# Performance work log

Measured on AMD Instinct MI355X. Metric: run time of the kernel, lower is better.

## Reference

```python
import jax, jax.numpy as jnp
import numpy as np

N, E = 20000, 320000
C, IN_NF, HID_NF, OUT_NF, CH_NF, RAD_NF = 14, 128, 128, 128, 16, 128
CONSTANT = 1.0
LN_EPS = 1e-5
SCALE = 0.02


def _pool_matrix(c, dtype):
    # RollerPooling buffer: pool_matrix[i] averages a sliding window of size c-i
    ones = np.ones((c, c), dtype=np.float32)
    mats = [(np.triu(ones) - np.triu(ones, k=c - i)) / float(c - i) for i in range(c)]
    return jnp.asarray(np.stack(mats), dtype=dtype)


def setup_inputs() -> dict:
    key = jax.random.key(0)
    ks = jax.random.split(key, 32)
    h = jax.random.normal(ks[0], (N, IN_NF), jnp.float32)
    x = jax.random.normal(ks[1], (N, C, 3), jnp.float32)
    row = jax.random.randint(ks[2], (E,), 0, N)
    off = jax.random.randint(ks[3], (E,), 1, N)
    col = (row + off) % N  # guarantees row != col (avoids zero-distance edges)
    channel_attr = jax.random.normal(ks[4], (N, C, CH_NF), jnp.float32)
    w = jax.random.uniform(ks[5], (N, C), jnp.float32, 0.1, 1.0)
    keep = jax.random.uniform(ks[6], (N, C)) > 0.3
    keep = keep.at[:, 0].set(True)  # every node has >=1 active channel
    channel_weights = w * keep.astype(jnp.float32)

    def lin(k, o, i):
        k1, k2 = jax.random.split(k)
        return (jax.random.normal(k1, (o, i), jnp.float32) * SCALE,
                jax.random.normal(k2, (o,), jnp.float32) * SCALE)

    radial_W, radial_b = lin(ks[7], RAD_NF, CH_NF * CH_NF)
    e1_W, e1_b = lin(ks[8], HID_NF, 2 * IN_NF + RAD_NF)
    e2_W, e2_b = lin(ks[9], HID_NF, HID_NF)
    att_W, att_b = lin(ks[10], 1, HID_NF)
    c1_W, c1_b = lin(ks[11], HID_NF, HID_NF)
    c2_W, c2_b = lin(ks[12], C, HID_NF)
    n1_W, n1_b = lin(ks[13], HID_NF, IN_NF + HID_NF)
    n2_W, n2_b = lin(ks[14], OUT_NF, HID_NF)
    ln_g = jnp.ones((OUT_NF,), jnp.float32)
    ln_b = jnp.zeros((OUT_NF,), jnp.float32)
    return dict(h=h, x=x, row=row, col=col, channel_attr=channel_attr,
                channel_weights=channel_weights,
                radial_W=radial_W, radial_b=radial_b,
                e1_W=e1_W, e1_b=e1_b, e2_W=e2_W, e2_b=e2_b,
                att_W=att_W, att_b=att_b,
                c1_W=c1_W, c1_b=c1_b, c2_W=c2_W, c2_b=c2_b,
                n1_W=n1_W, n1_b=n1_b, n2_W=n2_W, n2_b=n2_b,
                ln_g=ln_g, ln_b=ln_b)


def _scatter_mean(v, idx, n):
    s = jnp.zeros((n,) + v.shape[1:], v.dtype).at[idx].add(v)
    cnt = jnp.zeros((n,), v.dtype).at[idx].add(1.0)
    cnt = jnp.maximum(cnt, 1.0)
    return s / cnt.reshape((n,) + (1,) * (v.ndim - 1))


def _forward(h, x, row, col, channel_attr, channel_weights,
             radial_W, radial_b, e1_W, e1_b, e2_W, e2_b, att_W, att_b,
             c1_W, c1_b, c2_W, c2_b, n1_W, n1_b, n2_W, n2_b, ln_g, ln_b):
    n, c, d = x.shape
    silu = jax.nn.silu
    coord_r = x[row]           # [E, C, 3]
    coord_c = x[col]
    # pairwise channel distances [E, C, C]
    dist = jnp.linalg.norm(coord_r[:, :, None, :] - coord_c[:, None, :, :], axis=-1)
    cw_r = channel_weights[row]
    cw_c = channel_weights[col]
    coord_msg = dist * (cw_r[:, :, None] * cw_c[:, None, :])
    # attr_r^T @ coord_msg @ attr_c -> [E, CH_NF, CH_NF]
    radial = jnp.einsum('eca,ecd,edb->eab', channel_attr[row], coord_msg, channel_attr[col])
    radial = radial.reshape(radial.shape[0], -1)
    rnorm = jnp.linalg.norm(radial, axis=-1, keepdims=True) + CONSTANT
    radial = (radial @ radial_W.T + radial_b) / rnorm  # [E, RAD_NF]
    # pooled column coord over active channels
    mask = (channel_weights != 0).astype(x.dtype)      # [N, C]
    csum = mask.sum(-1)                                # [N]
    pooled_col = (coord_c * mask[col][:, :, None]).sum(1) / csum[col][:, None]  # [E, 3]
    coord_diff = coord_r - pooled_col[:, None, :]      # [E, C, 3]
    # edge MLP (dropout = identity in eval)
    ef = jnp.concatenate([h[row], h[col], radial], axis=-1)
    ef = silu(ef @ e1_W.T + e1_b)
    ef = silu(ef @ e2_W.T + e2_b)
    ef = ef * jax.nn.sigmoid(ef @ att_W.T + att_b)     # att_mlp (hidden_nf == input_nf)
    # coord MLP + roller pooling
    ch = silu(ef @ c1_W.T + c1_b) @ c2_W.T + c2_b      # [E, C]
    tsize = csum[row].astype(jnp.int32) - 1            # [E] in [0, C-1]
    pool_mat = _pool_matrix(c, x.dtype)                # [C, C, C]
    pooled = jnp.einsum('eij,ej->ei', pool_mat[tsize], ch)  # [E, C]
    trans = coord_diff * pooled[:, :, None]            # [E, C, 3]
    x_out = x + _scatter_mean(trans, row, n)
    agg = _scatter_mean(ef, col, n)
    nh = jnp.concatenate([h, agg], axis=-1)
    nh = silu(nh @ n1_W.T + n1_b) @ n2_W.T + n2_b
    y = h + nh
    mu = y.mean(-1, keepdims=True)
    var = ((y - mu) ** 2).mean(-1, keepdims=True)
    h_out = (y - mu) / jnp.sqrt(var + LN_EPS) * ln_g + ln_b
    return h_out, x_out


def reference(h, x, row, col, channel_attr, channel_weights,
              radial_W, radial_b, e1_W, e1_b, e2_W, e2_b, att_W, att_b,
              c1_W, c1_b, c2_W, c2_b, n1_W, n1_b, n2_W, n2_b, ln_g, ln_b):
    return _forward(h, x, row, col, channel_attr, channel_weights,
                    radial_W, radial_b, e1_W, e1_b, e2_W, e2_b, att_W, att_b,
                    c1_W, c1_b, c2_W, c2_b, n1_W, n1_b, n2_W, n2_b, ln_g, ln_b)
```

## Files before the change

### kernel.cpp

```cpp
#include <hip/hip_runtime.h>
#include <math.h>

#define NN 20000
#define NE 320000

typedef const float* fp;
typedef short short8 __attribute__((ext_vector_type(8)));
typedef short short4v __attribute__((ext_vector_type(4)));
typedef float f32x4 __attribute__((ext_vector_type(4)));

__device__ __forceinline__ short F2B(float f) {
    unsigned u = __float_as_uint(f);
    return (short)((u + 0x7fffu + ((u >> 16) & 1u)) >> 16);
}
__device__ __forceinline__ short F2Bf(float f) {
    return (short)((__float_as_uint(f) + 0x8000u) >> 16);
}
__device__ __forceinline__ float B2F(short s) {
    return __uint_as_float(((unsigned)(unsigned short)s) << 16);
}
__device__ __forceinline__ float siluf(float v) { return v / (1.f + __expf(-v)); }
__device__ __forceinline__ f32x4 ld4(const float* p) {
    f32x4 v;
    __builtin_memcpy(&v, p, 16);
    return v;
}

#if defined(__has_builtin)
#if __has_builtin(__builtin_amdgcn_mfma_f32_16x16x16bf16_1k)
#define MFMA16_BUILTIN 1
__device__ __forceinline__ f32x4 mfma16(short4v a, short4v b, f32x4 c) {
    return __builtin_amdgcn_mfma_f32_16x16x16bf16_1k(a, b, c, 0, 0, 0);
}
#elif __has_builtin(__builtin_amdgcn_mfma_f32_16x16x16_bf16)
#define MFMA16_BUILTIN 1
__device__ __forceinline__ f32x4 mfma16(short4v a, short4v b, f32x4 c) {
    return __builtin_amdgcn_mfma_f32_16x16x16_bf16(a, b, c, 0, 0, 0);
}
#endif
#endif
#ifndef MFMA16_BUILTIN
__device__ __forceinline__ f32x4 mfma16(short4v a, short4v b, f32x4 c) {
    f32x4 d;
    asm volatile("s_nop 1\n\tv_mfma_f32_16x16x16_bf16 %0, %1, %2, %3\n\ts_nop 7\n\ts_nop 7"
                 : "=v"(d) : "v"(a), "v"(b), "v"(c));
    return d;
}
#endif

__global__ void k_prep_w(fp e1W, fp e2W, fp c1W, fp c2W, fp n1W, fp n2W,
                         short* __restrict__ wb) {
    int i = blockIdx.x * 256 + threadIdx.x;
    if (i >= 149504) return;
    if (i >= 32768 && i < 65536) return;
    float v;
    if (i < 32768)       { int o = i >> 8, k = i & 255; v = e1W[o * 384 + k]; }
    else if (i < 81920)  v = e2W[i - 65536];
    else if (i < 98304)  v = c1W[i - 81920];
    else if (i < 100352) { int q = i - 98304; v = (q < 1792) ? c2W[q] : 0.f; }
    else if (i < 133120) v = n1W[i - 100352];
    else                 v = n2W[i - 133120];
    wb[i] = F2B(v);
}

__global__ void k_fold(fp e1W, fp rW, fp rB, short* __restrict__ wb,
                       float* __restrict__ bc) {
    int o = blockIdx.x, k = threadIdx.x;
    float acc = 0.f;
    for (int m = 0; m < 128; m++) acc += e1W[o * 384 + 256 + m] * rW[m * 256 + k];
    wb[32768 + o * 256 + k] = F2B(acc);
    if (k == 0) {
        float b = 0.f;
        for (int m = 0; m < 128; m++) b += e1W[o * 384 + 256 + m] * rB[m];
        bc[o] = b;
    }
}

__global__ void k_prep_h(fp h, short* __restrict__ hb) {
    int i = blockIdx.x * 256 + threadIdx.x;
    if (i < NN * 128) hb[i] = F2B(h[i]);
}

__global__ void k_prep_attrT(fp attr, fp cw, short* __restrict__ aT) {
    int i = blockIdx.x * 256 + threadIdx.x;
    if (i >= NN * 256) return;
    int n = i >> 8, rem = i & 255, c = rem >> 4, a = rem & 15;
    float v = (c < 14) ? attr[(size_t)n * 224 + c * 16 + a] * cw[n * 14 + c] : 0.f;
    aT[(size_t)n * 256 + a * 16 + c] = F2B(v);
}

__global__ void k_node_pre(fp x, fp cw, float* __restrict__ csum, float* __restrict__ pool) {
    int n = blockIdx.x * blockDim.x + threadIdx.x;
    if (n >= NN) return;
    float cnt = 0.f, px = 0.f, py = 0.f, pz = 0.f;
#pragma unroll
    for (int c = 0; c < 14; c++) {
        float w = cw[n * 14 + c];
        if (w != 0.f) {
            cnt += 1.f;
            px += x[(n * 14 + c) * 3 + 0];
            py += x[(n * 14 + c) * 3 + 1];
            pz += x[(n * 14 + c) * 3 + 2];
        }
    }
    if (cnt < 1.f) cnt = 1.f;
    csum[n] = cnt;
    pool[n * 3 + 0] = px / cnt;
    pool[n * 3 + 1] = py / cnt;
    pool[n * 3 + 2] = pz / cnt;
}

__global__ void k_prep_all(fp e1W, fp e2W, fp c1W, fp c2W, fp n1W, fp n2W,
                           fp rW, fp rB, fp h, fp x, fp attr, fp cw,
                           const int* __restrict__ row, const int* __restrict__ col,
                           short* __restrict__ wb, float* __restrict__ bc,
                           short* __restrict__ hb,
                           float* __restrict__ csum, float* __restrict__ pool,
                           short* __restrict__ aT,
                           int* __restrict__ cnt_r, int* __restrict__ cnt_c) {
    int b = blockIdx.x;
    const int tid = threadIdx.x;
    if (b < 1250) {
        int e = b * 256 + tid;
        if (e < NE) {
            atomicAdd(&cnt_c[col[e]], 1);
            atomicAdd(&cnt_r[row[e]], 1);
        }
        return;
    }
    b -= 1250;
    if (b < 584) {
        int i = b * 256 + tid;
        if (i >= 149504) return;
        if (i >= 32768 && i < 65536) return;
        float v;
        if (i < 32768)       { int o = i >> 8, k = i & 255; v = e1W[o * 384 + k]; }
        else if (i < 81920)  v = e2W[i - 65536];
        else if (i < 98304)  v = c1W[i - 81920];
        else if (i < 100352) { int q = i - 98304; v = (q < 1792) ? c2W[q] : 0.f; }
        else if (i < 133120) v = n1W[i - 100352];
        else                 v = n2W[i - 133120];
        wb[i] = F2B(v);
        return;
    }
    b -= 584;
    if (b < 128) {
        int o = b, k = tid;
        float acc = 0.f;
        for (int m = 0; m < 128; m++) acc += e1W[o * 384 + 256 + m] * rW[m * 256 + k];
        wb[32768 + o * 256 + k] = F2B(acc);
        if (k == 0) {
            float bsum = 0.f;
            for (int m = 0; m < 128; m++) bsum += e1W[o * 384 + 256 + m] * rB[m];
            bc[o] = bsum;
        }
        return;
    }
    b -= 128;
    if (b < 10000) {
        int i = b * 256 + tid;
        hb[i] = F2B(h[i]);
        return;
    }
    b -= 10000;
    if (b < 79) {
        int n = b * 256 + tid;
        if (n >= NN) return;
        float cnt = 0.f, px = 0.f, py = 0.f, pz = 0.f;
#pragma unroll
        for (int c = 0; c < 14; c++) {
            float w = cw[n * 14 + c];
            if (w != 0.f) {
                cnt += 1.f;
                px += x[(n * 14 + c) * 3 + 0];
                py += x[(n * 14 + c) * 3 + 1];
                pz += x[(n * 14 + c) * 3 + 2];
            }
        }
        if (cnt < 1.f) cnt = 1.f;
        csum[n] = cnt;
        pool[n * 3 + 0] = px / cnt;
        pool[n * 3 + 1] = py / cnt;
        pool[n * 3 + 2] = pz / cnt;
        return;
    }
    b -= 79;
    {
        int i = b * 256 + tid;
        int n = i >> 8, rem = i & 255, c = rem >> 4, a = rem & 15;
        float v = (c < 14) ? attr[(size_t)n * 224 + c * 16 + a] * cw[n * 14 + c] : 0.f;
        aT[(size_t)n * 256 + a * 16 + c] = F2B(v);
    }
}

__global__ void k_scan(int* __restrict__ cnt0, int* __restrict__ cnt1,
                       int* __restrict__ off0, int* __restrict__ off1) {
    __shared__ int part[256];
    const int tid = threadIdx.x;
    for (int a = 0; a < 2; a++) {
        int* cnt = a ? cnt1 : cnt0;
        int* off = a ? off1 : off0;
        int c0 = tid * 79, c1 = c0 + 79;
        if (c1 > 20000) c1 = 20000;
        int s = 0;
        for (int i = c0; i < c1; i++) s += cnt[i];
        part[tid] = s;
        __syncthreads();
        if (tid == 0) {
            int r = 0;
            for (int i = 0; i < 256; i++) { int t = part[i]; part[i] = r; r += t; }
        }
        __syncthreads();
        int run = part[tid];
        for (int i = c0; i < c1; i++) {
            int cv = cnt[i];
            off[i] = run;
            cnt[i] = run;
            run += cv;
        }
        if (tid == 255) off[20000] = run;
        __syncthreads();
    }
}

__global__ void k_fill(const int* __restrict__ row, const int* __restrict__ col,
                       int* __restrict__ head_r, int* __restrict__ head_c,
                       int* __restrict__ eidx_r,
                       int* __restrict__ row_s, int* __restrict__ col_s) {
    int e = blockIdx.x * 256 + threadIdx.x;
    if (e >= NE) return;
    int r = row[e], c = col[e];
    int pc = atomicAdd(&head_c[c], 1);
    row_s[pc] = r;
    col_s[pc] = c;
    int pr = atomicAdd(&head_r[r], 1);
    eidx_r[pr] = pc;
}

__device__ __forceinline__ void gemm_lds(const short* __restrict__ A, int sA,
                                         const short* __restrict__ W, int Ws, int K,
                                         int mt, int nt0, int nts, f32x4* acc) {
    const int lane = threadIdx.x & 63;
    const short* ap = A + (mt * 16 + (lane & 15)) * sA + ((lane >> 4) * 8);
    for (int k0 = 0; k0 < K; k0 += 32) {
        short8 a = *(const short8*)(ap + k0);
#pragma unroll
        for (int t = 0; t < nts; t++) {
            short8 b = *(const short8*)(W + ((nt0 + t) * 16 + (lane & 15)) * Ws + k0 + ((lane >> 4) * 8));
            acc[t] = __builtin_amdgcn_mfma_f32_16x16x32_bf16(a, b, acc[t], 0, 0, 0);
        }
    }
}
__device__ __forceinline__ void gemm_grow(const short* __restrict__ arow,
                                          const short* __restrict__ W, int Ws, int K,
                                          int nt0, int nts, f32x4* acc) {
    const int lane = threadIdx.x & 63;
    for (int k0 = 0; k0 < K; k0 += 32) {
        short8 a = *(const short8*)(arow + k0);
#pragma unroll
        for (int t = 0; t < nts; t++) {
            short8 b = *(const short8*)(W + ((nt0 + t) * 16 + (lane & 15)) * Ws + k0 + ((lane >> 4) * 8));
            acc[t] = __builtin_amdgcn_mfma_f32_16x16x32_bf16(a, b, acc[t], 0, 0, 0);
        }
    }
}

__global__ __launch_bounds__(256, 2) void k_hw(const short* __restrict__ hb,
                                               const short* __restrict__ wb,
                                               short* __restrict__ H12) {
    __shared__ __attribute__((aligned(16))) short A[32 * 136];
    const int tid = threadIdx.x, lane = tid & 63, w = tid >> 6;
    const int bb = lane & 15, quad = lane >> 4;
    const int mt = w & 1, nh = w >> 1, nb0 = blockIdx.x * 32;
    for (int p = tid; p < 512; p += 256) {
        int i = p >> 4, v = p & 15;
        *(short8*)(A + i * 136 + v * 8) = *(const short8*)(hb + (size_t)(nb0 + i) * 128 + v * 8);
    }
    __syncthreads();
    f32x4 acc[4];
#pragma unroll
    for (int t = 0; t < 4; t++) acc[t] = (f32x4){0.f, 0.f, 0.f, 0.f};
    gemm_lds(A, 136, wb, 256, 128, mt, nh * 4, 4, acc);
#pragma unroll
    for (int t = 0; t < 4; t++)
#pragma unroll
        for (int i = 0; i < 4; i++) {
            int m = mt * 16 + quad * 4 + i, n = (nh * 4 + t) * 16 + bb;
            H12[(size_t)(nb0 + m) * 256 + n] = F2Bf(acc[t][i]);
        }
#pragma unroll
    for (int t = 0; t < 4; t++) acc[t] = (f32x4){0.f, 0.f, 0.f, 0.f};
    gemm_lds(A, 136, wb + 128, 256, 128, mt, nh * 4, 4, acc);
#pragma unroll
    for (int t = 0; t < 4; t++)
#pragma unroll
        for (int i = 0; i < 4; i++) {
            int m = mt * 16 + quad * 4 + i, n = (nh * 4 + t) * 16 + bb;
            H12[(size_t)(nb0 + m) * 256 + 128 + n] = F2Bf(acc[t][i]);
        }
}

__global__ __launch_bounds__(256, 7) void k_edge(
    fp x, const int* __restrict__ row_s, const int* __restrict__ col_s,
    const short* __restrict__ attrT, const short* __restrict__ H12,
    const short* __restrict__ wb, const float* __restrict__ bc,
    fp e1B, fp e2B, fp aW, fp aB, fp c1B, fp c2B,
    const float* __restrict__ csum, const float* __restrict__ poolc,
    short* __restrict__ e1p, short* __restrict__ pooledb,
    float* __restrict__ pcrec) {
    __shared__ __attribute__((aligned(16))) short U[8704];
    __shared__ float s_inv[32];
    __shared__ int s_r[32], s_c[32];
    __shared__ float s_ch[32][14];
    __shared__ float s_red8[32][8], s_gate[32];

    const int tid = threadIdx.x, lane = tid & 63, w = tid >> 6;
    const int bb = lane & 15, quad = lane >> 4;
    const int mt = w & 1, nh = w >> 1;
    const int e0 = blockIdx.x * 32;
    const short* Wc = wb + 32768;
    short* Ar = U;
    short* V1 = U;
    short* V2 = U + 4352;

    if (tid < 32) { s_r[tid] = row_s[e0 + tid]; s_c[tid] = col_s[e0 + tid]; }
    __syncthreads();

    const int iic = bb < 14 ? bb : 13;
    const bool q3 = (quad == 3);
    const int cb = q3 ? 30 : quad * 12;
#pragma unroll 2
    for (int m = 0; m < 8; m++) {
        const int ei = w * 8 + m;
        const int r = s_r[ei], c = s_c[ei];
        short4v arv = *(const short4v*)(attrT + (size_t)r * 256 + bb * 16 + quad * 4);
        short4v acv = *(const short4v*)(attrT + (size_t)c * 256 + bb * 16 + quad * 4);
        const float* xrp = x + (size_t)r * 42 + iic * 3;
        float xr0 = xrp[0], xr1 = xrp[1], xr2 = xrp[2];
        const float* xcp = x + (size_t)c * 42 + cb;
        f32x4 L0 = ld4(xcp), L1 = ld4(xcp + 4), L2 = ld4(xcp + 8);
        float cxv[4], cyv[4], czv[4];
        cxv[0] = q3 ? L1[2] : L0[0]; cyv[0] = q3 ? L1[3] : L0[1]; czv[0] = q3 ? L2[0] : L0[2];
        cxv[1] = q3 ? L2[1] : L0[3]; cyv[1] = q3 ? L2[2] : L1[0]; czv[1] = q3 ? L2[3] : L1[1];
        cxv[2] = q3 ? L2[1] : L1[2]; cyv[2] = q3 ? L2[2] : L1[3]; czv[2] = q3 ? L2[3] : L2[0];
        cxv[3] = L2[1];              cyv[3] = L2[2];              czv[3] = L2[3];
        short4v msgv;
#pragma unroll
        for (int t = 0; t < 4; t++) {
            float dx = xr0 - cxv[t], dy = xr1 - cyv[t], dz = xr2 - czv[t];
            msgv[t] = F2Bf(sqrtf(dx * dx + dy * dy + dz * dz));
        }
        f32x4 t2 = mfma16(msgv, acv, (f32x4){0.f, 0.f, 0.f, 0.f});
        short4v t2v;
#pragma unroll
        for (int g = 0; g < 4; g++) t2v[g] = F2Bf(t2[g]);
        f32x4 rad = mfma16(arv, t2v, (f32x4){0.f, 0.f, 0.f, 0.f});
        float ss = rad[0] * rad[0] + rad[1] * rad[1] + rad[2] * rad[2] + rad[3] * rad[3];
#pragma unroll
        for (int off = 32; off > 0; off >>= 1) ss += __shfl_xor(ss, off, 64);
        float inv = 1.f / (sqrtf(ss) + 1.f);
        if (lane == 0) s_inv[ei] = inv;
#pragma unroll
        for (int g = 0; g < 4; g++)
            Ar[ei * 264 + (quad * 4 + g) * 16 + bb] = F2Bf(rad[g] * inv);
    }
    __syncthreads();

    f32x4 racc[2][2];
#pragma unroll
    for (int a = 0; a < 2; a++)
#pragma unroll
        for (int b = 0; b < 2; b++) racc[a][b] = (f32x4){0.f, 0.f, 0.f, 0.f};
    for (int k0 = 0; k0 < 256; k0 += 32) {
        short8 a0 = *(const short8*)(Ar + bb * 264 + k0 + quad * 8);
        short8 a1 = *(const short8*)(Ar + (16 + bb) * 264 + k0 + quad * 8);
        short8 b0 = *(const short8*)(Wc + (size_t)(w * 32 + bb) * 256 + k0 + quad * 8);
        short8 b1 = *(const short8*)(Wc + (size_t)(w * 32 + 16 + bb) * 256 + k0 + quad * 8);
        racc[0][0] = __builtin_amdgcn_mfma_f32_16x16x32_bf16(a0, b0, racc[0][0], 0, 0, 0);
        racc[0][1] = __builtin_amdgcn_mfma_f32_16x16x32_bf16(a0, b1, racc[0][1], 0, 0, 0);
        racc[1][0] = __builtin_amdgcn_mfma_f32_16x16x32_bf16(a1, b0, racc[1][0], 0, 0, 0);
        racc[1][1] = __builtin_amdgcn_mfma_f32_16x16x32_bf16(a1, b1, racc[1][1], 0, 0, 0);
    }
    __syncthreads();

#pragma unroll
    for (int a = 0; a < 2; a++)
#pragma unroll
        for (int b = 0; b < 2; b++)
#pragma unroll
            for (int i = 0; i < 4; i++) {
                int m = a * 16 + quad * 4 + i, n = w * 32 + b * 16 + bb;
                V1[m * 136 + n] = F2Bf(racc[a][b][i] + s_inv[m] * bc[n]);
            }
    __syncthreads();

    for (int p = tid; p < 512; p += 256) {
        int e = p >> 4, v = p & 15;
        short8 hr = *(const short8*)(H12 + (size_t)s_r[e] * 256 + v * 8);
        short8 hc = *(const short8*)(H12 + (size_t)s_c[e] * 256 + 128 + v * 8);
        short8 pp = *(const short8*)(V1 + e * 136 + v * 8);
        short8 o;
#pragma unroll
        for (int j = 0; j < 8; j++)
            o[j] = F2Bf(siluf(B2F(hr[j]) + B2F(hc[j]) + B2F(pp[j]) + e1B[v * 8 + j]));
        *(short8*)(V1 + e * 136 + v * 8) = o;
    }
    __syncthreads();

    f32x4 acc[4];
#pragma unroll
    for (int t = 0; t < 4; t++) acc[t] = (f32x4){0.f, 0.f, 0.f, 0.f};
    gemm_lds(V1, 136, wb + 65536, 128, 128, mt, nh * 4, 4, acc);
#pragma unroll
    for (int t = 0; t < 4; t++)
#pragma unroll
        for (int i = 0; i < 4; i++) {
            int m = mt * 16 + quad * 4 + i, n = (nh * 4 + t) * 16 + bb;
            V2[m * 136 + n] = F2Bf(siluf(acc[t][i] + e2B[n]));
        }
    __syncthreads();

    {
        int e = tid >> 3, j = tid & 7;
        float s = 0.f;
        for (int f = j * 16; f < j * 16 + 16; f++) s += B2F(V2[e * 136 + f]) * aW[f];
        s_red8[e][j] = s;
    }
    __syncthreads();
    if (tid < 32) {
        float s = 0.f;
#pragma unroll
        for (int j = 0; j < 8; j++) s += s_red8[tid][j];
        s_gate[tid] = 1.f / (1.f + __expf(-(s + aB[0])));
    }
#pragma unroll
    for (int t = 0; t < 4; t++) acc[t] = (f32x4){0.f, 0.f, 0.f, 0.f};
    gemm_lds(V2, 136, wb + 81920, 128, 128, mt, nh * 4, 4, acc);
    __syncthreads();

#pragma unroll
    for (int t = 0; t < 4; t++)
#pragma unroll
        for (int i = 0; i < 4; i++) {
            int m = mt * 16 + quad * 4 + i, n = (nh * 4 + t) * 16 + bb;
            V1[m * 136 + n] = F2Bf(siluf(s_gate[m] * acc[t][i] + c1B[n]));
        }
    for (int p = tid; p < 512; p += 256) {
        int e = p >> 4, v = p & 15;
        short8 a = *(const short8*)(V2 + e * 136 + v * 8);
        short8 o;
#pragma unroll
        for (int j = 0; j < 8; j++) o[j] = F2Bf(B2F(a[j]) * s_gate[e]);
        *(short8*)(e1p + (size_t)(e0 + e) * 128 + v * 8) = o;
    }
    __syncthreads();

    if (nh == 0) {
        f32x4 a4 = (f32x4){0.f, 0.f, 0.f, 0.f};
        gemm_lds(V1, 136, wb + 98304, 128, 128, mt, 0, 1, &a4);
#pragma unroll
        for (int i = 0; i < 4; i++) {
            int m = mt * 16 + quad * 4 + i;
            if (bb < 14) s_ch[m][bb] = a4[i] + c2B[bb];
        }
    }
    __syncthreads();

    if (tid < 32) {
        int t = (int)(csum[s_r[tid]] + 0.5f) - 1;
        if (t < 0) t = 0; if (t > 13) t = 13;
        int Wd = 14 - t;
        for (int i = 0; i < 14; i++) {
            int jend = i + Wd - 1; if (jend > 13) jend = 13;
            float a = 0.f;
            for (int j = i; j <= jend; j++) a += s_ch[tid][j];
            pooledb[(size_t)(e0 + tid) * 14 + i] = F2Bf(a / (float)Wd);
        }
        int c = s_c[tid];
        float4 pc = make_float4(poolc[c * 3 + 0], poolc[c * 3 + 1], poolc[c * 3 + 2], 0.f);
        *(float4*)(pcrec + (size_t)(e0 + tid) * 4) = pc;
    }
}

__global__ __launch_bounds__(256, 3) void k_edge_fused(
    fp x, const int* __restrict__ row, const int* __restrict__ col,
    fp attr, fp cw, const short* __restrict__ hb, const short* __restrict__ wb,
    fp e1B, fp e2B, fp aW, fp aB, fp c1B, fp c2B,
    const float* __restrict__ bc, const float* __restrict__ csum,
    const float* __restrict__ poolc,
    float* __restrict__ xacc, float* __restrict__ agg,
    float* __restrict__ cntr, float* __restrict__ cntc) {
    __shared__ __attribute__((aligned(16))) short R1[13056];
    __shared__ float s_xr2[32 * 42];
    __shared__ float T[4][352];
    __shared__ int   s_r[32], s_c[32];
    __shared__ float s_inv[32];
    __shared__ float s_ch[32][14], s_pool[32][14];
    __shared__ float s_red8[32][8];
    __shared__ float s_gate[32];

    const int tid = threadIdx.x, lane = tid & 63, w = tid >> 6;
    const int bb = lane & 15, quad = lane >> 4;

    if (tid < 32) { s_r[tid] = row[blockIdx.x * 32 + tid]; s_c[tid] = col[blockIdx.x * 32 + tid]; }
    __syncthreads();

    float* slot = T[w];
    float* t2w = slot + 72;
    for (int i8 = 0; i8 < 8; i8++) {
        const int e = w * 8 + i8;
        const int r = s_r[e], cl = s_c[e];
        if (lane < 42) {
            s_xr2[e * 42 + lane] = x[(size_t)r * 42 + lane];
            slot[lane] = x[(size_t)cl * 42 + lane];
        }
        if (lane < 14)      slot[42 + lane] = cw[r * 14 + lane];
        else if (lane < 28) slot[56 + (lane - 14)] = cw[cl * 14 + (lane - 14)];
        __builtin_amdgcn_wave_barrier();

        const int iic = bb < 14 ? bb : 13;
        float xr0 = s_xr2[e * 42 + iic * 3], xr1 = s_xr2[e * 42 + iic * 3 + 1],
              xr2v = s_xr2[e * 42 + iic * 3 + 2];
        float cwri = slot[42 + iic];
        short8 msgv, acv;
#pragma unroll
        for (int t = 0; t < 8; t++) {
            int jj = quad * 8 + t, jc = jj < 14 ? jj : 13;
            float dx = xr0 - slot[jc * 3], dy = xr1 - slot[jc * 3 + 1], dz = xr2v - slot[jc * 3 + 2];
            float m = sqrtf(dx * dx + dy * dy + dz * dz) * cwri * slot[56 + jc];
            msgv[t] = (bb < 14 && jj < 14) ? F2B(m) : (short)0;
            acv[t] = F2B(attr[(size_t)cl * 224 + jc * 16 + bb]);
        }
        f32x4 t2 = (f32x4){0.f, 0.f, 0.f, 0.f};
        t2 = __builtin_amdgcn_mfma_f32_16x16x32_bf16(msgv, acv, t2, 0, 0, 0);
#pragma unroll
        for (int g = 0; g < 4; g++) t2w[(quad * 4 + g) * 17 + bb] = t2[g];
        __builtin_amdgcn_wave_barrier();

        short8 arv, t2v;
#pragma unroll
        for (int t = 0; t < 8; t++) {
            int kk = quad * 8 + t, kc = kk < 16 ? kk : 15;
            t2v[t] = F2B(t2w[kc * 17 + bb]);
            arv[t] = (kk < 14) ? F2B(attr[(size_t)r * 224 + kk * 16 + bb]) : (short)0;
        }
        f32x4 rad = (f32x4){0.f, 0.f, 0.f, 0.f};
        rad = __builtin_amdgcn_mfma_f32_16x16x32_bf16(arv, t2v, rad, 0, 0, 0);

        float ss = rad[0] * rad[0] + rad[1] * rad[1] + rad[2] * rad[2] + rad[3] * rad[3];
#pragma unroll
        for (int off = 32; off > 0; off >>= 1) ss += __shfl_xor(ss, off, 64);
        float inv = 1.f / (sqrtf(ss) + 1.f);
        if (lane == 0) s_inv[e] = inv;
#pragma unroll
        for (int g = 0; g < 4; g++)
            R1[e * 264 + (quad * 4 + g) * 16 + bb] = F2B(rad[g] * inv);
        __builtin_amdgcn_wave_barrier();
    }
    __syncthreads();

    const int mt = w & 1, nh = w >> 1;
    const int m_ = mt * 16 + bb;
    f32x4 acc[4];
#pragma unroll
    for (int t = 0; t < 4; t++) acc[t] = (f32x4){0.f, 0.f, 0.f, 0.f};
    {
        const short* ar_ = hb + (size_t)s_r[m_] * 128 + quad * 8;
        const short* ac_ = hb + (size_t)s_c[m_] * 128 + quad * 8;
        gemm_grow(ar_, wb, 256, 128, nh * 4, 4, acc);
        gemm_grow(ac_, wb + 128, 256, 128, nh * 4, 4, acc);
        gemm_lds(R1, 264, wb + 32768, 256, 256, mt, nh * 4, 4, acc);
    }
    __syncthreads();
    short* V1 = R1;
    short* V2 = R1 + 4352;
    short* C1O = R1 + 8704;
#pragma unroll
    for (int t = 0; t < 4; t++)
#pragma unroll
        for (int i = 0; i < 4; i++) {
            int m = mt * 16 + quad * 4 + i, n = (nh * 4 + t) * 16 + bb;
            V1[m * 136 + n] = F2B(siluf(acc[t][i] + e1B[n] + bc[n] * s_inv[m]));
        }
    __syncthreads();

#pragma unroll
    for (int t = 0; t < 4; t++) acc[t] = (f32x4){0.f, 0.f, 0.f, 0.f};
    gemm_lds(V1, 136, wb + 65536, 128, 128, mt, nh * 4, 4, acc);
    __syncthreads();
#pragma unroll
    for (int t = 0; t < 4; t++)
#pragma unroll
        for (int i = 0; i < 4; i++) {
            int m = mt * 16 + quad * 4 + i, n = (nh * 4 + t) * 16 + bb;
            V2[m * 136 + n] = F2B(siluf(acc[t][i] + e2B[n]));
        }
    __syncthreads();

    {
        int e = tid >> 3, j = tid & 7;
        float s = 0.f;
        for (int f = j * 16; f < j * 16 + 16; f++) s += B2F(V2[e * 136 + f]) * aW[f];
        s_red8[e][j] = s;
    }
    __syncthreads();
    if (tid < 32) {
        float s = 0.f;
#pragma unroll
        for (int j = 0; j < 8; j++) s += s_red8[tid][j];
        s_gate[tid] = 1.f / (1.f + __expf(-(s + aB[0])));
    }
    __syncthreads();
    for (int p = tid; p < 32 * 128; p += 256) {
        int e = p >> 7, f = p & 127;
        V1[e * 136 + f] = F2B(B2F(V2[e * 136 + f]) * s_gate[e]);
    }
    __syncthreads();

#pragma unroll
    for (int t = 0; t < 4; t++) acc[t] = (f32x4){0.f, 0.f, 0.f, 0.f};
    gemm_lds(V1, 136, wb + 81920, 128, 128, mt, nh * 4, 4, acc);
    __syncthreads();
#pragma unroll
    for (int t = 0; t < 4; t++)
#pragma unroll
        for (int i = 0; i < 4; i++) {
            int m = mt * 16 + quad * 4 + i, n = (nh * 4 + t) * 16 + bb;
            C1O[m * 136 + n] = F2B(siluf(acc[t][i] + c1B[n]));
        }
    __syncthreads();

    if (nh == 0) {
        f32x4 a4 = (f32x4){0.f, 0.f, 0.f, 0.f};
        gemm_lds(C1O, 136, wb + 98304, 128, 128, mt, 0, 1, &a4);
#pragma unroll
        for (int i = 0; i < 4; i++) {
            int m = mt * 16 + quad * 4 + i;
            if (bb < 14) s_ch[m][bb] = a4[i] + c2B[bb];
        }
    }
    __syncthreads();

    if (tid < 32) {
        int t = (int)(csum[s_r[tid]] + 0.5f) - 1;
        if (t < 0) t = 0; if (t > 13) t = 13;
        int Wd = 14 - t;
        for (int i = 0; i < 14; i++) {
            int jend = i + Wd - 1; if (jend > 13) jend = 13;
            float a = 0.f;
            for (int j = i; j <= jend; j++) a += s_ch[tid][j];
            s_pool[tid][i] = a / (float)Wd;
        }
    }
    __syncthreads();

    for (int p = tid; p < 32 * 42; p += 256) {
        int e = p / 42, q = p - e * 42, i = q / 3, d = q - i * 3;
        float diff = s_xr2[e * 42 + q] - poolc[s_c[e] * 3 + d];
        atomicAdd(&xacc[(size_t)s_r[e] * 42 + q], diff * s_pool[e][i]);
    }
    for (int p = tid; p < 32 * 128; p += 256) {
        int e = p >> 7, f = p & 127;
        atomicAdd(&agg[(size_t)s_c[e] * 128 + f], B2F(V1[e * 136 + f]));
    }
    if (tid < 32) {
        atomicAdd(&cntr[s_r[tid]], 1.f);
        atomicAdd(&cntc[s_c[tid]], 1.f);
    }
}

__global__ __launch_bounds__(256, 4) void k_node_post_csr(
    fp h, fp x, const short* __restrict__ wb,
    fp n1B, fp n2B, fp lng, fp lnb,
    const short* __restrict__ efb, const short* __restrict__ pooledb,
    const int* __restrict__ off_c, const int* __restrict__ off_r,
    const int* __restrict__ eidx_r, const float* __restrict__ pcrec,
    float* __restrict__ outh, float* __restrict__ outx) {
    __shared__ __attribute__((aligned(16))) short nA[32 * 264];
    __shared__ __attribute__((aligned(16))) short nMid[32 * 136];
    __shared__ float nred8[32][8];
    __shared__ float nmu[32], nrs[32];
    float* nY = (float*)nA;

    const int tid = threadIdx.x;
    const int wave = tid >> 6, mt = wave & 1, nh = wave >> 1;
    const int lane = tid & 63, bb = lane & 15, quad = lane >> 4;
    const int nb0 = blockIdx.x * 32;
    const short* n1Wb = wb + 100352;
    const short* n2Wb = wb + 133120;

    for (int p = tid; p < 32 * 128; p += 256) {
        int i = p >> 7, f = p & 127;
        nA[i * 264 + f] = F2Bf(h[(size_t)(nb0 + i) * 128 + f]);
    }
    {
        const int ni = tid >> 3, seg = tid & 7;
        const int n = nb0 + ni;
        const int beg = off_c[n], end = off_c[n + 1];
        float av[16];
#pragma unroll
        for (int j = 0; j < 16; j++) av[j] = 0.f;
        for (int k = beg; k < end; k++) {
            short8 u0 = *(const short8*)(efb + (size_t)k * 128 + seg * 16);
            short8 u1 = *(const short8*)(efb + (size_t)k * 128 + seg * 16 + 8);
#pragma unroll
            for (int j = 0; j < 8; j++) { av[j] += B2F(u0[j]); av[8 + j] += B2F(u1[j]); }
        }
        float inv = 1.f / fmaxf((float)(end - beg), 1.f);
#pragma unroll
        for (int j = 0; j < 16; j++)
            nA[ni * 264 + 128 + seg * 16 + j] = F2Bf(av[j] * inv);
    }
    __syncthreads();

    f32x4 acc[4];
#pragma unroll
    for (int t = 0; t < 4; t++) acc[t] = (f32x4){0.f, 0.f, 0.f, 0.f};
    gemm_lds(nA, 264, n1Wb, 256, 256, mt, nh * 4, 4, acc);
#pragma unroll
    for (int t = 0; t < 4; t++)
#pragma unroll
        for (int i = 0; i < 4; i++) {
            int m = mt * 16 + quad * 4 + i, n = (nh * 4 + t) * 16 + bb;
            nMid[m * 136 + n] = F2Bf(siluf(acc[t][i] + n1B[n]));
        }
    __syncthreads();

#pragma unroll
    for (int t = 0; t < 4; t++) acc[t] = (f32x4){0.f, 0.f, 0.f, 0.f};
    gemm_lds(nMid, 136, n2Wb, 128, 128, mt, nh * 4, 4, acc);
#pragma unroll
    for (int t = 0; t < 4; t++)
#pragma unroll
        for (int i = 0; i < 4; i++) {
            int m = mt * 16 + quad * 4 + i, n = (nh * 4 + t) * 16 + bb;
            nY[m * 128 + n] = acc[t][i] + n2B[n] + h[(size_t)(nb0 + m) * 128 + n];
        }
    __syncthreads();

    {
        int i = tid >> 3, j = tid & 7;
        float s = 0.f;
        for (int f = j * 16; f < j * 16 + 16; f++) s += nY[i * 128 + f];
        nred8[i][j] = s;
    }
    __syncthreads();
    if (tid < 32) {
        float s = 0.f;
#pragma unroll
        for (int j = 0; j < 8; j++) s += nred8[tid][j];
        nmu[tid] = s * (1.f / 128.f);
    }
    __syncthreads();
    {
        int i = tid >> 3, j = tid & 7;
        float mu = nmu[i], s = 0.f;
        for (int f = j * 16; f < j * 16 + 16; f++) { float d = nY[i * 128 + f] - mu; s += d * d; }
        nred8[i][j] = s;
    }
    __syncthreads();
    if (tid < 32) {
        float s = 0.f;
#pragma unroll
        for (int j = 0; j < 8; j++) s += nred8[tid][j];
        nrs[tid] = rsqrtf(s * (1.f / 128.f) + 1e-5f);
    }
    __syncthreads();
    for (int p = tid; p < 32 * 128; p += 256) {
        int i = p >> 7, f = p & 127;
        outh[(size_t)(nb0 + i) * 128 + f] = (nY[i * 128 + f] - nmu[i]) * nrs[i] * lng[f] + lnb[f];
    }
    for (int p = tid; p < 32 * 3; p += 256) {
        int i = p / 3, d = p - i * 3;
        int n = nb0 + i;
        int beg = off_r[n], end = off_r[n + 1];
        float Q[14], P[14];
#pragma unroll
        for (int ic = 0; ic < 14; ic++) { Q[ic] = 0.f; P[ic] = 0.f; }
        for (int k = beg; k < end; k++) {
            int sp = eidx_r[k];
            const int* pp = (const int*)(pooledb + (size_t)sp * 14);
            float4 pc = *(const float4*)(pcrec + (size_t)sp * 4);
            float pcd = (d == 0) ? pc.x : ((d == 1) ? pc.y : pc.z);
#pragma unroll
            for (int u2 = 0; u2 < 7; u2++) {
                int u = pp[u2];
                float pw0 = B2F((short)(u & 0xffff));
                float pw1 = B2F((short)(((unsigned)u) >> 16));
                P[2 * u2] += pw0;     Q[2 * u2] += pw0 * pcd;
                P[2 * u2 + 1] += pw1; Q[2 * u2 + 1] += pw1 * pcd;
            }
        }
        float invd = 1.f / fmaxf((float)(end - beg), 1.f);
#pragma unroll
        for (int ic = 0; ic < 14; ic++) {
            float x0 = x[(size_t)n * 42 + ic * 3 + d];
            outx[(size_t)n * 42 + ic * 3 + d] = x0 + (x0 * P[ic] - Q[ic]) * invd;
        }
    }
}

__global__ __launch_bounds__(256, 2) void k_node_post(
    fp h, fp x, const short* __restrict__ wb,
    fp n1B, fp n2B, fp lng, fp lnb,
    const float* __restrict__ agg, const float* __restrict__ cntc,
    const float* __restrict__ xacc, const float* __restrict__ cntr,
    float* __restrict__ outh, float* __restrict__ outx) {
    __shared__ __attribute__((aligned(16))) short nA[32 * 264];
    __shared__ __attribute__((aligned(16))) short nMid[32 * 136];
    __shared__ float nY[32][128];
    __shared__ float nred8[32][8];
    __shared__ float nmu[32], nrs[32];

    const int tid = threadIdx.x;
    const int wave = tid >> 6, mt = wave & 1, nh = wave >> 1;
    const int lane = tid & 63, bb = lane & 15, quad = lane >> 4;
    const int nb0 = blockIdx.x * 32;
    const short* n1Wb = wb + 100352;
    const short* n2Wb = wb + 133120;

    for (int p = tid; p < 32 * 128; p += 256) {
        int i = p >> 7, f = p & 127;
        int n = nb0 + i;
        nA[i * 264 + f] = F2Bf(h[(size_t)n * 128 + f]);
        float cc = cntc[n]; if (cc < 1.f) cc = 1.f;
        nA[i * 264 + 128 + f] = F2Bf(agg[(size_t)n * 128 + f] / cc);
    }
    __syncthreads();

    f32x4 acc[4];
#pragma unroll
    for (int t = 0; t < 4; t++) acc[t] = (f32x4){0.f, 0.f, 0.f, 0.f};
    gemm_lds(nA, 264, n1Wb, 256, 256, mt, nh * 4, 4, acc);
#pragma unroll
    for (int t = 0; t < 4; t++)
#pragma unroll
        for (int i = 0; i < 4; i++) {
            int m = mt * 16 + quad * 4 + i, n = (nh * 4 + t) * 16 + bb;
            nMid[m * 136 + n] = F2Bf(siluf(acc[t][i] + n1B[n]));
        }
    __syncthreads();

#pragma unroll
    for (int t = 0; t < 4; t++) acc[t] = (f32x4){0.f, 0.f, 0.f, 0.f};
    gemm_lds(nMid, 136, n2Wb, 128, 128, mt, nh * 4, 4, acc);
#pragma unroll
    for (int t = 0; t < 4; t++)
#pragma unroll
        for (int i = 0; i < 4; i++) {
            int m = mt * 16 + quad * 4 + i, n = (nh * 4 + t) * 16 + bb;
            nY[m][n] = acc[t][i] + n2B[n] + h[(size_t)(nb0 + m) * 128 + n];
        }
    __syncthreads();

    {
        int i = tid >> 3, j = tid & 7;
        float s = 0.f;
        for (int f = j * 16; f < j * 16 + 16; f++) s += nY[i][f];
        nred8[i][j] = s;
    }
    __syncthreads();
    if (tid < 32) {
        float s = 0.f;
#pragma unroll
        for (int j = 0; j < 8; j++) s += nred8[tid][j];
        nmu[tid] = s * (1.f / 128.f);
    }
    __syncthreads();
    {
        int i = tid >> 3, j = tid & 7;
        float mu = nmu[i], s = 0.f;
        for (int f = j * 16; f < j * 16 + 16; f++) { float d = nY[i][f] - mu; s += d * d; }
        nred8[i][j] = s;
    }
    __syncthreads();
    if (tid < 32) {
        float s = 0.f;
#pragma unroll
        for (int j = 0; j < 8; j++) s += nred8[tid][j];
        nrs[tid] = rsqrtf(s * (1.f / 128.f) + 1e-5f);
    }
    __syncthreads();
    for (int p = tid; p < 32 * 128; p += 256) {
        int i = p >> 7, f = p & 127;
        outh[(size_t)(nb0 + i) * 128 + f] = (nY[i][f] - nmu[i]) * nrs[i] * lng[f] + lnb[f];
    }
    for (int p = tid; p < 32 * 42; p += 256) {
        int i = p / 42, q = p - i * 42;
        int n = nb0 + i;
        float cr = cntr[n]; if (cr < 1.f) cr = 1.f;
        outx[(size_t)n * 42 + q] = x[(size_t)n * 42 + q] + xacc[(size_t)n * 42 + q] / cr;
    }
}

extern "C" void kernel_launch(void* const* d_in, const int* in_sizes, int n_in,
                              void* d_out, int out_size, void* d_ws, size_t ws_size,
                              hipStream_t stream) {
    fp h   = (fp)d_in[0];
    fp x   = (fp)d_in[1];
    const int* row = (const int*)d_in[2];
    const int* col = (const int*)d_in[3];
    fp attr= (fp)d_in[4];
    fp cw  = (fp)d_in[5];
    fp rW  = (fp)d_in[6];  fp rB  = (fp)d_in[7];
    fp e1W = (fp)d_in[8];  fp e1B = (fp)d_in[9];
    fp e2W = (fp)d_in[10]; fp e2B = (fp)d_in[11];
    fp aW  = (fp)d_in[12]; fp aB  = (fp)d_in[13];
    fp c1W = (fp)d_in[14]; fp c1B = (fp)d_in[15];
    fp c2W = (fp)d_in[16]; fp c2B = (fp)d_in[17];
    fp n1W = (fp)d_in[18]; fp n1B = (fp)d_in[19];
    fp n2W = (fp)d_in[20]; fp n2B = (fp)d_in[21];
    fp lng = (fp)d_in[22]; fp lnb = (fp)d_in[23];

    float* ws    = (float*)d_ws;
    int*   wsi   = (int*)d_ws;
    float* xacc  = ws;
    float* agg   = ws + 840000;
    float* cntr  = ws + 3400000;
    float* cntc  = ws + 3420000;
    float* csum  = ws + 3440000;
    float* pool  = ws + 3460000;
    float* bc    = ws + 3520000;
    short* hb    = (short*)(ws + 3520128);
    short* wb    = (short*)(ws + 4800128);
    short* H12   = (short*)(ws + 4874880);
    short* e1p   = (short*)(ws + 7434880);
    short* attrT = (short*)(ws + 27914880);
    short* pooledb = (short*)(ws + 1040004);
    float* pcrec   = ws + 3520128;

    int* off_c  = wsi + 0;
    int* off_r  = wsi + 20002;
    int* head_c = wsi + 40004;
    int* head_r = wsi + 60004;
    int* eidx_r = wsi + 80004;
    int* row_s  = wsi + 400004;
    int* col_s  = wsi + 720004;

    const size_t need = 30474880ull * 4ull;

    if (ws_size >= need) {
        hipMemsetAsync(head_c, 0, 40000 * sizeof(int), stream);
        k_prep_all<<<32041, 256, 0, stream>>>(e1W, e2W, c1W, c2W, n1W, n2W,
                                              rW, rB, h, x, attr, cw, row, col,
                                              wb, bc, hb, csum, pool, attrT,
                                              head_r, head_c);
        k_scan<<<1, 256, 0, stream>>>(head_c, head_r, off_c, off_r);
        k_fill<<<(NE + 255) / 256, 256, 0, stream>>>(row, col, head_r, head_c,
                                                     eidx_r, row_s, col_s);
        k_hw<<<NN / 32, 256, 0, stream>>>(hb, wb, H12);
        k_edge<<<NE / 32, 256, 0, stream>>>(x, row_s, col_s, attrT, H12, wb, bc,
                                            e1B, e2B, aW, aB, c1B, c2B,
                                            csum, pool, e1p, pooledb, pcrec);
        float* outh = (float*)d_out;
        float* outx = outh + NN * 128;
        k_node_post_csr<<<NN / 32, 256, 0, stream>>>(h, x, wb, n1B, n2B, lng, lnb,
                                                     e1p, pooledb,
                                                     off_c, off_r, eidx_r,
                                                     pcrec, outh, outx);
    } else {
        hipMemsetAsync(d_ws, 0, 3440000 * sizeof(float), stream);
        k_prep_w<<<(149504 + 255) / 256, 256, 0, stream>>>(e1W, e2W, c1W, c2W, n1W, n2W, wb);
        k_fold<<<128, 256, 0, stream>>>(e1W, rW, rB, wb, bc);
        k_prep_h<<<(NN * 128 + 255) / 256, 256, 0, stream>>>(h, hb);
        k_node_pre<<<(NN + 255) / 256, 256, 0, stream>>>(x, cw, csum, pool);
        k_edge_fused<<<NE / 32, 256, 0, stream>>>(x, row, col, attr, cw, hb, wb,
                                                  e1B, e2B, aW, aB, c1B, c2B,
                                                  bc, csum, pool, xacc, agg, cntr, cntc);
        float* outh = (float*)d_out;
        float* outx = outh + NN * 128;
        k_node_post<<<NN / 32, 256, 0, stream>>>(h, x, wb, n1B, n2B, lng, lnb,
                                                 agg, cntc, xacc, cntr, outh, outx);
    }
}
```

Measured before the change: 686.6 us.

## Scatter pooled outputs to row-sorted positions and use prefix sums for pooling

k_fill now records each edge's row-sorted position instead of an indirection index, and k_edge writes pooledb and pcrec directly at that position. The node post kernel can then read them contiguously by row without a per-edge indirect load. The sliding-window pooling is computed from a prefix sum instead of a nested loop, and k_hw launch bounds are raised to allow more occupancy. In exchange, the writes in k_edge become scattered.

```diff
diff --git a/kernel.cpp b/kernel.cpp
--- a/kernel.cpp
+++ b/kernel.cpp
@@ -225,7 +225,7 @@
 
 __global__ void k_fill(const int* __restrict__ row, const int* __restrict__ col,
                        int* __restrict__ head_r, int* __restrict__ head_c,
-                       int* __restrict__ eidx_r,
+                       int* __restrict__ rpos,
                        int* __restrict__ row_s, int* __restrict__ col_s) {
     int e = blockIdx.x * 256 + threadIdx.x;
     if (e >= NE) return;
@@ -234,7 +234,7 @@
     row_s[pc] = r;
     col_s[pc] = c;
     int pr = atomicAdd(&head_r[r], 1);
-    eidx_r[pr] = pc;
+    rpos[pc] = pr;
 }
 
 __device__ __forceinline__ void gemm_lds(const short* __restrict__ A, int sA,
@@ -265,7 +265,7 @@
     }
 }
 
-__global__ __launch_bounds__(256, 2) void k_hw(const short* __restrict__ hb,
+__global__ __launch_bounds__(256, 4) void k_hw(const short* __restrict__ hb,
                                                const short* __restrict__ wb,
                                                short* __restrict__ H12) {
     __shared__ __attribute__((aligned(16))) short A[32 * 136];
@@ -302,6 +302,7 @@
 
 __global__ __launch_bounds__(256, 7) void k_edge(
     fp x, const int* __restrict__ row_s, const int* __restrict__ col_s,
+    const int* __restrict__ rpos,
     const short* __restrict__ attrT, const short* __restrict__ H12,
     const short* __restrict__ wb, const float* __restrict__ bc,
     fp e1B, fp e2B, fp aW, fp aB, fp c1B, fp c2B,
@@ -312,6 +313,7 @@
     __shared__ float s_inv[32];
     __shared__ int s_r[32], s_c[32];
     __shared__ float s_ch[32][14];
+    __shared__ float s_ps[32][15];
     __shared__ float s_red8[32][8], s_gate[32];
 
     const int tid = threadIdx.x, lane = tid & 63, w = tid >> 6;
@@ -470,15 +472,18 @@
         int t = (int)(csum[s_r[tid]] + 0.5f) - 1;
         if (t < 0) t = 0; if (t > 13) t = 13;
         int Wd = 14 - t;
+        float run = 0.f;
+        s_ps[tid][0] = 0.f;
+        for (int j = 0; j < 14; j++) { run += s_ch[tid][j]; s_ps[tid][j + 1] = run; }
+        float invW = 1.f / (float)Wd;
+        int rp = rpos[e0 + tid];
         for (int i = 0; i < 14; i++) {
-            int jend = i + Wd - 1; if (jend > 13) jend = 13;
-            float a = 0.f;
-            for (int j = i; j <= jend; j++) a += s_ch[tid][j];
-            pooledb[(size_t)(e0 + tid) * 14 + i] = F2Bf(a / (float)Wd);
+            int jend = i + Wd; if (jend > 14) jend = 14;
+            pooledb[(size_t)rp * 14 + i] = F2Bf((s_ps[tid][jend] - s_ps[tid][i]) * invW);
         }
         int c = s_c[tid];
         float4 pc = make_float4(poolc[c * 3 + 0], poolc[c * 3 + 1], poolc[c * 3 + 2], 0.f);
-        *(float4*)(pcrec + (size_t)(e0 + tid) * 4) = pc;
+        *(float4*)(pcrec + (size_t)rp * 4) = pc;
     }
 }
 
@@ -674,7 +679,7 @@
     fp n1B, fp n2B, fp lng, fp lnb,
     const short* __restrict__ efb, const short* __restrict__ pooledb,
     const int* __restrict__ off_c, const int* __restrict__ off_r,
-    const int* __restrict__ eidx_r, const float* __restrict__ pcrec,
+    const float* __restrict__ pcrec,
     float* __restrict__ outh, float* __restrict__ outx) {
     __shared__ __attribute__((aligned(16))) short nA[32 * 264];
     __shared__ __attribute__((aligned(16))) short nMid[32 * 136];
@@ -778,9 +783,8 @@
 #pragma unroll
         for (int ic = 0; ic < 14; ic++) { Q[ic] = 0.f; P[ic] = 0.f; }
         for (int k = beg; k < end; k++) {
-            int sp = eidx_r[k];
-            const int* pp = (const int*)(pooledb + (size_t)sp * 14);
-            float4 pc = *(const float4*)(pcrec + (size_t)sp * 4);
+            const int* pp = (const int*)(pooledb + (size_t)k * 14);
+            float4 pc = *(const float4*)(pcrec + (size_t)k * 4);
             float pcd = (d == 0) ? pc.x : ((d == 1) ? pc.y : pc.z);
 #pragma unroll
             for (int u2 = 0; u2 < 7; u2++) {
@@ -933,7 +937,7 @@
     int* off_r  = wsi + 20002;
     int* head_c = wsi + 40004;
     int* head_r = wsi + 60004;
-    int* eidx_r = wsi + 80004;
+    int* rpos   = wsi + 80004;
     int* row_s  = wsi + 400004;
     int* col_s  = wsi + 720004;
 
@@ -947,16 +951,16 @@
                                               head_r, head_c);
         k_scan<<<1, 256, 0, stream>>>(head_c, head_r, off_c, off_r);
         k_fill<<<(NE + 255) / 256, 256, 0, stream>>>(row, col, head_r, head_c,
-                                                     eidx_r, row_s, col_s);
+                                                     rpos, row_s, col_s);
         k_hw<<<NN / 32, 256, 0, stream>>>(hb, wb, H12);
-        k_edge<<<NE / 32, 256, 0, stream>>>(x, row_s, col_s, attrT, H12, wb, bc,
+        k_edge<<<NE / 32, 256, 0, stream>>>(x, row_s, col_s, rpos, attrT, H12, wb, bc,
                                             e1B, e2B, aW, aB, c1B, c2B,
                                             csum, pool, e1p, pooledb, pcrec);
         float* outh = (float*)d_out;
         float* outx = outh + NN * 128;
         k_node_post_csr<<<NN / 32, 256, 0, stream>>>(h, x, wb, n1B, n2B, lng, lnb,
                                                      e1p, pooledb,
-                                                     off_c, off_r, eidx_r,
+                                                     off_c, off_r,
                                                      pcrec, outh, outx);
     } else {
         hipMemsetAsync(d_ws, 0, 3440000 * sizeof(float), stream);
```

Result: faster. 659.6 us (-3.9%).
